# Optimization experiments

Measured on AMD Instinct MI355X. Metric: run time of the kernel, lower is better.

Reference implementation:

```python
import jax, jax.numpy as jnp
import numpy as np

B, T, IN, H, GAT_HEADS, MHA_HEADS, C = 32, 512, 128, 256, 4, 4, 8
OUT = H // GAT_HEADS          # 64, GAT per-head out_features
HD = H // MHA_HEADS           # 64, MHA head dim
ALPHA = 0.2                   # LeakyReLU slope
EPS = 1e-5                    # LayerNorm eps


def setup_inputs() -> dict:
    key = jax.random.key(0)
    ks = iter(jax.random.split(key, 32))
    def rn(shape, scale=0.05):
        return jax.random.normal(next(ks), shape, dtype=jnp.float32) * scale
    return {
        "x": jax.random.normal(next(ks), (B, T, IN), dtype=jnp.float32),
        # GRU layer 0 / 1 (PyTorch gate order r,z,n)
        "gru_W_ih0": rn((3 * H, IN)), "gru_W_hh0": rn((3 * H, H)),
        "gru_b_ih0": rn((3 * H,)), "gru_b_hh0": rn((3 * H,)),
        "gru_W_ih1": rn((3 * H, H)), "gru_W_hh1": rn((3 * H, H)),
        "gru_b_ih1": rn((3 * H,)), "gru_b_hh1": rn((3 * H,)),
        # GAT: per-head W [H,OUT] and additive attention vector a [2*OUT]
        "gat_W": rn((GAT_HEADS, H, OUT)), "gat_a": rn((GAT_HEADS, 2 * OUT)),
        "ln_g": jnp.ones((H,), jnp.float32), "ln_b": jnp.zeros((H,), jnp.float32),
        # MHA packed in-proj (q,k,v) + out-proj
        "mha_in_w": rn((3 * H, H)), "mha_in_b": rn((3 * H,)),
        "mha_out_w": rn((H, H)), "mha_out_b": rn((H,)),
        "fc1_w": rn((H // 2, H)), "fc1_b": rn((H // 2,)),
        "fc2_w": rn((C, H // 2)), "fc2_b": rn((C,)),
    }


def _gru_layer(x, W_ih, W_hh, b_ih, b_hh):
    # x: [B,T,D] -> hidden states [B,T,H]; PyTorch GRU cell math, gates r,z,n
    xp = jnp.einsum('btd,gd->btg', x, W_ih) + b_ih  # precompute input proj [B,T,3H]
    Hh = W_hh.shape[1]
    def step(h, xp_t):
        g = h @ W_hh.T + b_hh
        xr, xz, xn = jnp.split(xp_t, 3, axis=-1)
        hr, hz, hn = jnp.split(g, 3, axis=-1)
        r = jax.nn.sigmoid(xr + hr)
        z = jax.nn.sigmoid(xz + hz)
        n = jnp.tanh(xn + r * hn)
        h_new = (1.0 - z) * n + z * h
        return h_new, h_new
    h0 = jnp.zeros((x.shape[0], Hh), x.dtype)
    _, hs = jax.lax.scan(step, h0, jnp.swapaxes(xp, 0, 1))
    return jnp.swapaxes(hs, 0, 1)


def _gat_head(h_in, W, a):
    # Additive attention decomposed: e_ij = leakyrelu(a1.h_i + a2.h_j)
    # (exactly equals matmul(cat[h_i,h_j], a) without the [B,T,T,2*OUT] tensor)
    h = h_in @ W                       # [B,T,OUT]
    f_src = h @ a[:OUT]                # [B,T]
    f_dst = h @ a[OUT:]                # [B,T]
    e = jax.nn.leaky_relu(f_src[:, :, None] + f_dst[:, None, :], ALPHA)  # [B,T,T]
    attn = jax.nn.softmax(e, axis=-1)  # dropout is identity in eval mode
    return jnp.einsum('bij,bjd->bid', attn, h)


def _layer_norm(x, g, b):
    mu = x.mean(-1, keepdims=True)
    var = jnp.mean((x - mu) ** 2, -1, keepdims=True)
    return (x - mu) * jax.lax.rsqrt(var + EPS) * g + b


def _forward(x, gru_W_ih0, gru_W_hh0, gru_b_ih0, gru_b_hh0,
             gru_W_ih1, gru_W_hh1, gru_b_ih1, gru_b_hh1,
             gat_W, gat_a, ln_g, ln_b,
             mha_in_w, mha_in_b, mha_out_w, mha_out_b,
             fc1_w, fc1_b, fc2_w, fc2_b):
    g = _gru_layer(x, gru_W_ih0, gru_W_hh0, gru_b_ih0, gru_b_hh0)
    g = _gru_layer(g, gru_W_ih1, gru_W_hh1, gru_b_ih1, gru_b_hh1)  # [B,T,H]
    gat_out = jnp.concatenate([_gat_head(g, gat_W[i], gat_a[i]) for i in range(GAT_HEADS)], axis=-1)
    y = _layer_norm(g + gat_out, ln_g, ln_b)
    # Multihead self-attention (4 heads, eval-mode dropout = identity)
    qkv = y @ mha_in_w.T + mha_in_b
    q, k, v = jnp.split(qkv, 3, axis=-1)
    def split_heads(t):
        return t.reshape(t.shape[0], t.shape[1], MHA_HEADS, HD).transpose(0, 2, 1, 3)
    q, k, v = split_heads(q), split_heads(k), split_heads(v)
    scores = jnp.einsum('bhqd,bhkd->bhqk', q, k) / jnp.sqrt(jnp.float32(HD))
    attn = jax.nn.softmax(scores, axis=-1)
    ctx = jnp.einsum('bhqk,bhkd->bhqd', attn, v)
    ctx = ctx.transpose(0, 2, 1, 3).reshape(y.shape[0], y.shape[1], H)
    attn_out = ctx @ mha_out_w.T + mha_out_b
    pooled = attn_out.mean(axis=1)                    # [B,H]
    hid = jax.nn.relu(pooled @ fc1_w.T + fc1_b)
    return hid @ fc2_w.T + fc2_b                      # [B,C]


def reference(x, gru_W_ih0, gru_W_hh0, gru_b_ih0, gru_b_hh0,
              gru_W_ih1, gru_W_hh1, gru_b_ih1, gru_b_hh1,
              gat_W, gat_a, ln_g, ln_b,
              mha_in_w, mha_in_b, mha_out_w, mha_out_b,
              fc1_w, fc1_b, fc2_w, fc2_b):
    return _forward(x, gru_W_ih0, gru_W_hh0, gru_b_ih0, gru_b_hh0,
                    gru_W_ih1, gru_W_hh1, gru_b_ih1, gru_b_hh1,
                    gat_W, gat_a, ln_g, ln_b,
                    mha_in_w, mha_in_b, mha_out_w, mha_out_b,
                    fc1_w, fc1_b, fc2_w, fc2_b)
```

## Files before the change

kernel.cpp:

```cpp
#include <hip/hip_runtime.h>
#include <math.h>

#define BB 32
#define TT 512
#define INF_ 128
#define HH 256
#define H3 768
#define NHEADS 4
#define HDIM 64

typedef _Float16 half_t;
typedef half_t half2_t __attribute__((ext_vector_type(2)));
typedef half_t half4_t __attribute__((ext_vector_type(4)));
typedef half_t f16x8 __attribute__((ext_vector_type(8)));
typedef float f32x4 __attribute__((ext_vector_type(4)));

#if defined(__has_builtin)
#if __has_builtin(__builtin_amdgcn_fdot2)
#define FDOT2(a, b, c) __builtin_amdgcn_fdot2((a), (b), (c), false)
#endif
#endif
#ifndef FDOT2
#define FDOT2(a, b, c) fmaf((float)(a).x, (float)(b).x, fmaf((float)(a).y, (float)(b).y, (c)))
#endif

#define BCH(x) __builtin_bit_cast(half2_t, x)
#define PKH(a, b) __builtin_bit_cast(unsigned, half2_t{(half_t)(a), (half_t)(b)})

__device__ __forceinline__ float wsum(float v) {
#pragma unroll
  for (int o = 32; o > 0; o >>= 1) v += __shfl_xor(v, o, 64);
  return v;
}
__device__ __forceinline__ float wmax(float v) {
#pragma unroll
  for (int o = 32; o > 0; o >>= 1) v = fmaxf(v, __shfl_xor(v, o, 64));
  return v;
}

__global__ void castk(const float* __restrict__ s, half_t* __restrict__ d, int n) {
  int i = (blockIdx.x * 256 + threadIdx.x) * 4;
  if (i < n) {
    float4 v = *(const float4*)(s + i);
    half4_t o = {(half_t)v.x, (half_t)v.y, (half_t)v.z, (half_t)v.w};
    *(half4_t*)(d + i) = o;
  }
}

__global__ __launch_bounds__(256) void gemm_f16(
    const half_t* __restrict__ A, const half_t* __restrict__ B,
    const float* __restrict__ bias, float* __restrict__ C,
    int M, int N, int K) {
  __shared__ __align__(16) half_t As[128][40];
  __shared__ __align__(16) half_t Bs[64][40];
  const int tid = threadIdx.x;
  const int wave = tid >> 6, lane = tid & 63;
  const int m0 = blockIdx.y * 128, n0 = blockIdx.x * 64;
  const int mrow = lane & 15, quad = lane >> 4;
  f32x4 acc00 = {0.f, 0.f, 0.f, 0.f}, acc01 = acc00, acc02 = acc00, acc03 = acc00;
  f32x4 acc10 = acc00, acc11 = acc00, acc12 = acc00, acc13 = acc00;
  for (int k0 = 0; k0 < K; k0 += 32) {
    __syncthreads();
#pragma unroll
    for (int u = 0; u < 2; ++u) {
      int idx = tid + u * 256;
      int row = idx >> 2, seg = idx & 3;
      *(f16x8*)&As[row][seg * 8] =
          *(const f16x8*)&A[(size_t)(m0 + row) * K + k0 + seg * 8];
    }
    {
      int row = tid >> 2, seg = tid & 3;
      *(f16x8*)&Bs[row][seg * 8] =
          *(const f16x8*)&B[(size_t)(n0 + row) * K + k0 + seg * 8];
    }
    __syncthreads();
    f16x8 af0 = *(const f16x8*)&As[wave * 32 + mrow][quad * 8];
    f16x8 af1 = *(const f16x8*)&As[wave * 32 + 16 + mrow][quad * 8];
    f16x8 bf0 = *(const f16x8*)&Bs[mrow][quad * 8];
    f16x8 bf1 = *(const f16x8*)&Bs[16 + mrow][quad * 8];
    f16x8 bf2 = *(const f16x8*)&Bs[32 + mrow][quad * 8];
    f16x8 bf3 = *(const f16x8*)&Bs[48 + mrow][quad * 8];
    acc00 = __builtin_amdgcn_mfma_f32_16x16x32_f16(af0, bf0, acc00, 0, 0, 0);
    acc01 = __builtin_amdgcn_mfma_f32_16x16x32_f16(af0, bf1, acc01, 0, 0, 0);
    acc02 = __builtin_amdgcn_mfma_f32_16x16x32_f16(af0, bf2, acc02, 0, 0, 0);
    acc03 = __builtin_amdgcn_mfma_f32_16x16x32_f16(af0, bf3, acc03, 0, 0, 0);
    acc10 = __builtin_amdgcn_mfma_f32_16x16x32_f16(af1, bf0, acc10, 0, 0, 0);
    acc11 = __builtin_amdgcn_mfma_f32_16x16x32_f16(af1, bf1, acc11, 0, 0, 0);
    acc12 = __builtin_amdgcn_mfma_f32_16x16x32_f16(af1, bf2, acc12, 0, 0, 0);
    acc13 = __builtin_amdgcn_mfma_f32_16x16x32_f16(af1, bf3, acc13, 0, 0, 0);
  }
  float bv0 = bias ? bias[n0 + mrow] : 0.f;
  float bv1 = bias ? bias[n0 + 16 + mrow] : 0.f;
  float bv2 = bias ? bias[n0 + 32 + mrow] : 0.f;
  float bv3 = bias ? bias[n0 + 48 + mrow] : 0.f;
  const int rb = m0 + wave * 32 + quad * 4;
#pragma unroll
  for (int r = 0; r < 4; ++r) {
    float* c0 = C + (size_t)(rb + r) * N + n0;
    c0[mrow] = acc00[r] + bv0;
    c0[16 + mrow] = acc01[r] + bv1;
    c0[32 + mrow] = acc02[r] + bv2;
    c0[48 + mrow] = acc03[r] + bv3;
    float* c1 = C + (size_t)(rb + 16 + r) * N + n0;
    c1[mrow] = acc10[r] + bv0;
    c1[16 + mrow] = acc11[r] + bv1;
    c1[32 + mrow] = acc12[r] + bv2;
    c1[48 + mrow] = acc13[r] + bv3;
  }
}

#define LDW(g, p, a, b, i)                             \
  {                                                    \
    float4 v = (p)[i];                                 \
    g##a = half2_t{(half_t)v.x, (half_t)v.y};          \
    g##b = half2_t{(half_t)v.z, (half_t)v.w};          \
  }
#define LDW28(g, p)                                                        \
  LDW(g, p, 0, 1, 0) LDW(g, p, 2, 3, 1) LDW(g, p, 4, 5, 2)                 \
  LDW(g, p, 6, 7, 3) LDW(g, p, 8, 9, 4) LDW(g, p, 10, 11, 5)               \
  LDW(g, p, 12, 13, 6) LDW(g, p, 14, 15, 7) LDW(g, p, 16, 17, 8)           \
  LDW(g, p, 18, 19, 9) LDW(g, p, 20, 21, 10) LDW(g, p, 22, 23, 11)         \
  LDW(g, p, 24, 25, 12) LDW(g, p, 26, 27, 13) LDW(g, p, 28, 29, 14)        \
  LDW(g, p, 30, 31, 15) LDW(g, p, 32, 33, 16) LDW(g, p, 34, 35, 17)        \
  LDW(g, p, 36, 37, 18) LDW(g, p, 38, 39, 19) LDW(g, p, 40, 41, 20)        \
  LDW(g, p, 42, 43, 21) LDW(g, p, 44, 45, 22) LDW(g, p, 46, 47, 23)        \
  LDW(g, p, 48, 49, 24) LDW(g, p, 50, 51, 25) LDW(g, p, 52, 53, 26)        \
  LDW(g, p, 54, 55, 27)

#define DECL56(g)                                                          \
  half2_t g##0, g##1, g##2, g##3, g##4, g##5, g##6, g##7, g##8, g##9,      \
      g##10, g##11, g##12, g##13, g##14, g##15, g##16, g##17, g##18,       \
      g##19, g##20, g##21, g##22, g##23, g##24, g##25, g##26, g##27,       \
      g##28, g##29, g##30, g##31, g##32, g##33, g##34, g##35, g##36,       \
      g##37, g##38, g##39, g##40, g##41, g##42, g##43, g##44, g##45,       \
      g##46, g##47, g##48, g##49, g##50, g##51, g##52, g##53, g##54, g##55;

#define CHA(c8, a0, a1, a2, a3)                                            \
  {                                                                        \
    float4 v = hp4[c8];                                                    \
    uint4 nv = WSq[((c8)-1) * 512 + tid];                                  \
    half2_t t0 = __builtin_bit_cast(half2_t, v.x);                         \
    half2_t t1 = __builtin_bit_cast(half2_t, v.y);                         \
    half2_t t2 = __builtin_bit_cast(half2_t, v.z);                         \
    half2_t t3 = __builtin_bit_cast(half2_t, v.w);                         \
    ar = FDOT2(wr##a0, t0, ar); az = FDOT2(wz##a0, t0, az); an = FDOT2(BCH(nv.x), t0, an); \
    ar = FDOT2(wr##a1, t1, ar); az = FDOT2(wz##a1, t1, az); an = FDOT2(BCH(nv.y), t1, an); \
    ar = FDOT2(wr##a2, t2, ar); az = FDOT2(wz##a2, t2, az); an = FDOT2(BCH(nv.z), t2, an); \
    ar = FDOT2(wr##a3, t3, ar); az = FDOT2(wz##a3, t3, az); an = FDOT2(BCH(nv.w), t3, an); \
  }

#define CHB(c8)                                                            \
  {                                                                        \
    float4 v = hp4[c8];                                                    \
    uint4 nv = WSq[((c8)-1) * 512 + tid];                                  \
    uint4 rv = WSq[(15 + ((c8)-14)) * 512 + tid];                          \
    uint4 zv = WSq[(17 + ((c8)-14)) * 512 + tid];                          \
    half2_t t0 = __builtin_bit_cast(half2_t, v.x);                         \
    half2_t t1 = __builtin_bit_cast(half2_t, v.y);                         \
    half2_t t2 = __builtin_bit_cast(half2_t, v.z);                         \
    half2_t t3 = __builtin_bit_cast(half2_t, v.w);                         \
    ar = FDOT2(BCH(rv.x), t0, ar); az = FDOT2(BCH(zv.x), t0, az); an = FDOT2(BCH(nv.x), t0, an); \
    ar = FDOT2(BCH(rv.y), t1, ar); az = FDOT2(BCH(zv.y), t1, az); an = FDOT2(BCH(nv.y), t1, an); \
    ar = FDOT2(BCH(rv.z), t2, ar); az = FDOT2(BCH(zv.z), t2, az); an = FDOT2(BCH(nv.z), t2, an); \
    ar = FDOT2(BCH(rv.w), t3, ar); az = FDOT2(BCH(zv.w), t3, az); an = FDOT2(BCH(nv.w), t3, an); \
  }

__global__ __launch_bounds__(512) void gru_layer(
    const float* __restrict__ xp, const float* __restrict__ Whh,
    const float* __restrict__ bhh, float* __restrict__ out,
    half_t* __restrict__ out16) {
  __shared__ __align__(16) uint4 WSq[19 * 512];
  __shared__ __align__(16) half_t hs[2][2][144];
  const int tid = threadIdx.x;
  const int kh = tid & 1, j = tid >> 1;
  const int b = blockIdx.x;
  DECL56(wr)
  DECL56(wz)
  half2_t wn0, wn1, wn2, wn3;
  {
    const float4* pr = (const float4*)(Whh + (size_t)j * HH + kh * 128);
    const float4* pz = (const float4*)(Whh + (size_t)(HH + j) * HH + kh * 128);
    const float4* pn = (const float4*)(Whh + (size_t)(2 * HH + j) * HH + kh * 128);
    LDW28(wr, pr)
    LDW28(wz, pz)
    LDW(wn, pn, 0, 1, 0)
    LDW(wn, pn, 2, 3, 1)
  }
  {
    const float* rowN = Whh + (size_t)(2 * HH + j) * HH + kh * 128;
    const float* rowR = Whh + (size_t)j * HH + kh * 128;
    const float* rowZ = Whh + (size_t)(HH + j) * HH + kh * 128;
#pragma unroll
    for (int sg = 0; sg < 15; ++sg) {
      float2 g0 = *(const float2*)(rowN + (4 * sg + 4) * 2);
      float2 g1 = *(const float2*)(rowN + (4 * sg + 5) * 2);
      float2 g2 = *(const float2*)(rowN + (4 * sg + 6) * 2);
      float2 g3 = *(const float2*)(rowN + (4 * sg + 7) * 2);
      WSq[sg * 512 + tid] =
          uint4{PKH(g0.x, g0.y), PKH(g1.x, g1.y), PKH(g2.x, g2.y), PKH(g3.x, g3.y)};
    }
#pragma unroll
    for (int sg = 0; sg < 2; ++sg) {
      float2 g0 = *(const float2*)(rowR + (56 + 4 * sg) * 2);
      float2 g1 = *(const float2*)(rowR + (57 + 4 * sg) * 2);
      float2 g2 = *(const float2*)(rowR + (58 + 4 * sg) * 2);
      float2 g3 = *(const float2*)(rowR + (59 + 4 * sg) * 2);
      WSq[(15 + sg) * 512 + tid] =
          uint4{PKH(g0.x, g0.y), PKH(g1.x, g1.y), PKH(g2.x, g2.y), PKH(g3.x, g3.y)};
    }
#pragma unroll
    for (int sg = 0; sg < 2; ++sg) {
      float2 g0 = *(const float2*)(rowZ + (56 + 4 * sg) * 2);
      float2 g1 = *(const float2*)(rowZ + (57 + 4 * sg) * 2);
      float2 g2 = *(const float2*)(rowZ + (58 + 4 * sg) * 2);
      float2 g3 = *(const float2*)(rowZ + (59 + 4 * sg) * 2);
      WSq[(17 + sg) * 512 + tid] =
          uint4{PKH(g0.x, g0.y), PKH(g1.x, g1.y), PKH(g2.x, g2.y), PKH(g3.x, g3.y)};
    }
  }
  const float br = bhh[j], bz = bhh[HH + j], bn = bhh[2 * HH + j];
  for (int i = tid; i < 288; i += 512) ((unsigned*)hs)[i] = 0u;
  __syncthreads();
  float hprev = 0.f;
  const float* xrow = xp + (size_t)b * TT * H3;
  float* orow = out + (size_t)b * TT * HH;
  half_t* orow16 = out16 + (size_t)b * TT * HH;
  for (int t = 0; t < TT; ++t) {
    float xr = xrow[j], xz = xrow[HH + j], xn = xrow[2 * HH + j];
    const float4* hp4 = (const float4*)&hs[t & 1][kh][0];
    float ar = 0.f, az = 0.f, an = 0.f;
    {
      float4 v = hp4[0];
      half2_t t0 = __builtin_bit_cast(half2_t, v.x);
      half2_t t1 = __builtin_bit_cast(half2_t, v.y);
      half2_t t2 = __builtin_bit_cast(half2_t, v.z);
      half2_t t3 = __builtin_bit_cast(half2_t, v.w);
      ar = FDOT2(wr0, t0, ar); az = FDOT2(wz0, t0, az); an = FDOT2(wn0, t0, an);
      ar = FDOT2(wr1, t1, ar); az = FDOT2(wz1, t1, az); an = FDOT2(wn1, t1, an);
      ar = FDOT2(wr2, t2, ar); az = FDOT2(wz2, t2, az); an = FDOT2(wn2, t2, an);
      ar = FDOT2(wr3, t3, ar); az = FDOT2(wz3, t3, az); an = FDOT2(wn3, t3, an);
    }
    CHA(1, 4, 5, 6, 7)
    CHA(2, 8, 9, 10, 11)
    CHA(3, 12, 13, 14, 15)
    CHA(4, 16, 17, 18, 19)
    CHA(5, 20, 21, 22, 23)
    CHA(6, 24, 25, 26, 27)
    CHA(7, 28, 29, 30, 31)
    CHA(8, 32, 33, 34, 35)
    CHA(9, 36, 37, 38, 39)
    CHA(10, 40, 41, 42, 43)
    CHA(11, 44, 45, 46, 47)
    CHA(12, 48, 49, 50, 51)
    CHA(13, 52, 53, 54, 55)
    CHB(14)
    CHB(15)
    ar += __shfl_xor(ar, 1);
    az += __shfl_xor(az, 1);
    an += __shfl_xor(an, 1);
    float rg = 1.f / (1.f + __expf(-(xr + ar + br)));
    float zg = 1.f / (1.f + __expf(-(xz + az + bz)));
    float ng = 2.f / (1.f + __expf(-2.f * (xn + rg * (an + bn)))) - 1.f;
    float hnew = (1.f - zg) * ng + zg * hprev;
    hprev = hnew;
    float hpart = __shfl_xor(hnew, 2);
    if ((tid & 3) == 0) {
      half2_t pk;
      pk.x = (half_t)hnew;
      pk.y = (half_t)hpart;
      *(half2_t*)&hs[(t + 1) & 1][j >> 7][j & 127] = pk;
    }
    if (kh == 0) {
      orow[j] = hnew;
      orow16[j] = (half_t)hnew;
    }
    __syncthreads();
    xrow += H3;
    orow += HH;
    orow16 += HH;
  }
}

__global__ void gat_wt(const float* __restrict__ W, half_t* __restrict__ Wt) {
  int idx = blockIdx.x * 256 + threadIdx.x;
  int col = idx >> 8, k = idx & 255;
  Wt[idx] = (half_t)W[((size_t)((col >> 6) * HH + k)) * HDIM + (col & 63)];
}

__global__ void gat_fsd(const float* __restrict__ hgat, const float* __restrict__ a,
                        float* __restrict__ fsrc, float* __restrict__ fdst) {
  int b = blockIdx.x, hd = blockIdx.y, t = threadIdx.x;
  const float* hp = hgat + ((size_t)(b * TT + t)) * HH + hd * HDIM;
  const float* ap = a + hd * 2 * HDIM;
  float fs = 0.f, fd = 0.f;
#pragma unroll 4
  for (int d = 0; d < HDIM; ++d) {
    float hv = hp[d];
    fs += hv * ap[d];
    fd += hv * ap[HDIM + d];
  }
  fsrc[(b * NHEADS + hd) * TT + t] = fs;
  fdst[(b * NHEADS + hd) * TT + t] = fd;
}

__global__ __launch_bounds__(256) void gat_attn(
    const float* __restrict__ hgat, const float* __restrict__ fsrc,
    const float* __restrict__ fdst, float* __restrict__ out) {
  __shared__ __align__(16) float Ht[128][64];
  __shared__ __align__(16) float fd[128];
  __shared__ __align__(16) float pq[4][128][8];
  const int tid = threadIdx.x, wave = tid >> 6, lane = tid & 63;
  const int hd = blockIdx.y, b = blockIdx.z;
  const int i0 = blockIdx.x * 32 + wave * 8;
  const float* fs = fsrc + (size_t)(b * NHEADS + hd) * TT;
  const float* fdp = fdst + (size_t)(b * NHEADS + hd) * TT;
  float m[8], l[8], acc[8], fi[8];
#pragma unroll
  for (int q = 0; q < 8; ++q) { m[q] = -1e30f; l[q] = 0.f; acc[q] = 0.f; fi[q] = fs[i0 + q]; }
  for (int jt = 0; jt < TT; jt += 128) {
#pragma unroll
    for (int u = 0; u < 8; ++u) {
      int idx = tid + u * 256;
      int jj = idx >> 4, dq = (idx & 15) * 4;
      *(float4*)&Ht[jj][dq] =
          *(const float4*)&hgat[((size_t)(b * TT + jt + jj)) * HH + hd * HDIM + dq];
    }
    if (tid < 128) fd[tid] = fdp[jt + tid];
    __syncthreads();
#pragma unroll
    for (int q = 0; q < 8; ++q) {
      float e0 = fi[q] + fd[lane];      e0 = (e0 > 0.f) ? e0 : 0.2f * e0;
      float e1 = fi[q] + fd[lane + 64]; e1 = (e1 > 0.f) ? e1 : 0.2f * e1;
      float mn = fmaxf(m[q], wmax(fmaxf(e0, e1)));
      float corr = __expf(m[q] - mn);
      float p0 = __expf(e0 - mn), p1 = __expf(e1 - mn);
      l[q] = l[q] * corr + wsum(p0 + p1);
      m[q] = mn;
      acc[q] *= corr;
      pq[wave][lane][q] = p0;
      pq[wave][lane + 64][q] = p1;
    }
#pragma unroll 4
    for (int jj = 0; jj < 128; ++jj) {
      float4 pa = *(const float4*)&pq[wave][jj][0];
      float4 pb = *(const float4*)&pq[wave][jj][4];
      float hv = Ht[jj][lane];
      acc[0] += pa.x * hv; acc[1] += pa.y * hv; acc[2] += pa.z * hv; acc[3] += pa.w * hv;
      acc[4] += pb.x * hv; acc[5] += pb.y * hv; acc[6] += pb.z * hv; acc[7] += pb.w * hv;
    }
    __syncthreads();
  }
#pragma unroll
  for (int q = 0; q < 8; ++q)
    out[((size_t)(b * TT + i0 + q)) * HH + hd * HDIM + lane] = acc[q] / l[q];
}

__global__ __launch_bounds__(256) void ln_res(
    const float* __restrict__ g, const float* __restrict__ gat,
    const float* __restrict__ gamma, const float* __restrict__ beta,
    half_t* __restrict__ y16) {
  int wave = threadIdx.x >> 6, lane = threadIdx.x & 63;
  size_t n = (size_t)blockIdx.x * 4 + wave;
  float4 v = ((const float4*)(g + n * HH))[lane];
  float4 w = ((const float4*)(gat + n * HH))[lane];
  v.x += w.x; v.y += w.y; v.z += w.z; v.w += w.w;
  float mu = wsum(v.x + v.y + v.z + v.w) * (1.f / 256.f);
  float dx = v.x - mu, dy = v.y - mu, dz = v.z - mu, dw = v.w - mu;
  float var = wsum(dx * dx + dy * dy + dz * dz + dw * dw) * (1.f / 256.f);
  float rstd = rsqrtf(var + 1e-5f);
  float4 gm = ((const float4*)gamma)[lane];
  float4 bt = ((const float4*)beta)[lane];
  half4_t o = {(half_t)(dx * rstd * gm.x + bt.x), (half_t)(dy * rstd * gm.y + bt.y),
               (half_t)(dz * rstd * gm.z + bt.z), (half_t)(dw * rstd * gm.w + bt.w)};
  ((half4_t*)(y16 + n * HH))[lane] = o;
}

__global__ __launch_bounds__(256) void mha_attn(const float* __restrict__ qkv,
                                                half_t* __restrict__ ctx16) {
  __shared__ __align__(16) float KV[8320];
  __shared__ __align__(16) float qq[4][64][8];
  __shared__ __align__(16) float pq[4][128][8];
  const int tid = threadIdx.x, wave = tid >> 6, lane = tid & 63;
  const int hd = blockIdx.y, b = blockIdx.z;
  const int i0 = blockIdx.x * 32 + wave * 8;
#pragma unroll
  for (int q = 0; q < 8; ++q)
    qq[wave][lane][q] = qkv[((size_t)(b * TT + i0 + q)) * H3 + hd * HDIM + lane];
  float m[8], l[8], acc[8];
#pragma unroll
  for (int q = 0; q < 8; ++q) { m[q] = -1e30f; l[q] = 0.f; acc[q] = 0.f; }
  for (int jt = 0; jt < TT; jt += 128) {
#pragma unroll
    for (int u = 0; u < 8; ++u) {
      int idx = tid + u * 256;
      int jj = idx >> 4, dq = (idx & 15) * 4;
      float4 kv = *(const float4*)&qkv[((size_t)(b * TT + jt + jj)) * H3 + HH + hd * HDIM + dq];
      KV[(dq + 0) * 130 + jj] = kv.x;
      KV[(dq + 1) * 130 + jj] = kv.y;
      KV[(dq + 2) * 130 + jj] = kv.z;
      KV[(dq + 3) * 130 + jj] = kv.w;
    }
    __syncthreads();
    float e0[8] = {}, e1[8] = {};
#pragma unroll 8
    for (int dd = 0; dd < 64; ++dd) {
      float4 qa = *(const float4*)&qq[wave][dd][0];
      float4 qb = *(const float4*)&qq[wave][dd][4];
      float k0 = KV[dd * 130 + lane], k1 = KV[dd * 130 + 64 + lane];
      e0[0] += qa.x * k0; e0[1] += qa.y * k0; e0[2] += qa.z * k0; e0[3] += qa.w * k0;
      e0[4] += qb.x * k0; e0[5] += qb.y * k0; e0[6] += qb.z * k0; e0[7] += qb.w * k0;
      e1[0] += qa.x * k1; e1[1] += qa.y * k1; e1[2] += qa.z * k1; e1[3] += qa.w * k1;
      e1[4] += qb.x * k1; e1[5] += qb.y * k1; e1[6] += qb.z * k1; e1[7] += qb.w * k1;
    }
    __syncthreads();
#pragma unroll
    for (int u = 0; u < 8; ++u) {
      int idx = tid + u * 256;
      int jj = idx >> 4, dq = (idx & 15) * 4;
      *(float4*)&KV[jj * 64 + dq] =
          *(const float4*)&qkv[((size_t)(b * TT + jt + jj)) * H3 + 2 * HH + hd * HDIM + dq];
    }
#pragma unroll
    for (int q = 0; q < 8; ++q) {
      float s0 = e0[q] * 0.125f, s1 = e1[q] * 0.125f;
      float mn = fmaxf(m[q], wmax(fmaxf(s0, s1)));
      float corr = __expf(m[q] - mn);
      float p0 = __expf(s0 - mn), p1 = __expf(s1 - mn);
      l[q] = l[q] * corr + wsum(p0 + p1);
      m[q] = mn;
      acc[q] *= corr;
      pq[wave][lane][q] = p0;
      pq[wave][lane + 64][q] = p1;
    }
    __syncthreads();
#pragma unroll 4
    for (int jj = 0; jj < 128; ++jj) {
      float4 pa = *(const float4*)&pq[wave][jj][0];
      float4 pb = *(const float4*)&pq[wave][jj][4];
      float hv = KV[jj * 64 + lane];
      acc[0] += pa.x * hv; acc[1] += pa.y * hv; acc[2] += pa.z * hv; acc[3] += pa.w * hv;
      acc[4] += pb.x * hv; acc[5] += pb.y * hv; acc[6] += pb.z * hv; acc[7] += pb.w * hv;
    }
    __syncthreads();
  }
#pragma unroll
  for (int q = 0; q < 8; ++q)
    ctx16[((size_t)(b * TT + i0 + q)) * HH + hd * HDIM + lane] = (half_t)(acc[q] / l[q]);
}

__global__ void mean_pool(const float* __restrict__ x, float* __restrict__ out) {
  int b = blockIdx.x, j = threadIdx.x;
  const float* p = x + (size_t)b * TT * HH + j;
  float s = 0.f;
  for (int t = 0; t < TT; ++t) s += p[(size_t)t * HH];
  out[b * HH + j] = s * (1.f / 512.f);
}

__global__ void fc1_k(const float* __restrict__ pooled, const float* __restrict__ w,
                      const float* __restrict__ bias, float* __restrict__ hid) {
  int b = blockIdx.x, o = threadIdx.x;
  const float* pp = pooled + b * HH;
  const float* wp = w + o * HH;
  float s = 0.f;
#pragma unroll 4
  for (int k = 0; k < HH; ++k) s += pp[k] * wp[k];
  hid[b * 128 + o] = fmaxf(s + bias[o], 0.f);
}

__global__ void fc2_k(const float* __restrict__ hid, const float* __restrict__ w,
                      const float* __restrict__ bias, float* __restrict__ out) {
  int t = threadIdx.x;
  int mm = t >> 3, c = t & 7;
  const float* hp = hid + mm * 128;
  const float* wp = w + c * 128;
  float s = 0.f;
#pragma unroll 4
  for (int k = 0; k < 128; ++k) s += hp[k] * wp[k];
  out[mm * 8 + c] = s + bias[c];
}

extern "C" void kernel_launch(void* const* d_in, const int* in_sizes, int n_in,
                              void* d_out, int out_size, void* d_ws, size_t ws_size,
                              hipStream_t stream) {
  (void)in_sizes; (void)n_in; (void)out_size; (void)ws_size;
  const float* x    = (const float*)d_in[0];
  const float* Wih0 = (const float*)d_in[1];
  const float* Whh0 = (const float*)d_in[2];
  const float* bih0 = (const float*)d_in[3];
  const float* bhh0 = (const float*)d_in[4];
  const float* Wih1 = (const float*)d_in[5];
  const float* Whh1 = (const float*)d_in[6];
  const float* bih1 = (const float*)d_in[7];
  const float* bhh1 = (const float*)d_in[8];
  const float* gatW = (const float*)d_in[9];
  const float* gatA = (const float*)d_in[10];
  const float* lng  = (const float*)d_in[11];
  const float* lnb  = (const float*)d_in[12];
  const float* inw  = (const float*)d_in[13];
  const float* inb  = (const float*)d_in[14];
  const float* outw = (const float*)d_in[15];
  const float* outb = (const float*)d_in[16];
  const float* f1w  = (const float*)d_in[17];
  const float* f1b  = (const float*)d_in[18];
  const float* f2w  = (const float*)d_in[19];
  const float* f2b  = (const float*)d_in[20];
  float* out = (float*)d_out;
  float* ws = (float*)d_ws;

  float* XPA   = ws;
  float* G0    = ws + 12582912;
  float* G1    = G0 + 4194304;
  float* Yb    = G1 + 4194304;
  float* HGAT  = Yb + 4194304;
  float* GATWTf= HGAT + 4194304;
  float* FSRC  = GATWTf + 65536;
  float* FDST  = FSRC + 65536;
  float* POOL  = FDST + 65536;
  float* HIDb  = POOL + 8192;
  float* W16b  = HIDb + 4096;

  half_t* X16     = (half_t*)G1;
  half_t* G0_16   = (half_t*)Yb;
  half_t* G1_16   = (half_t*)(Yb + 2097152);
  half_t* CTX16   = (half_t*)HGAT;
  half_t* Y16     = (half_t*)(HGAT + 2097152);
  half_t* GATWT16 = (half_t*)GATWTf;
  half_t* W16ih0  = (half_t*)W16b;
  half_t* W16ih1  = (half_t*)(W16b + 49152);
  half_t* W16in   = (half_t*)(W16b + 49152 + 98304);
  half_t* W16out  = (half_t*)(W16b + 49152 + 98304 + 98304);

  castk<<<2048, 256, 0, stream>>>(x, X16, 2097152);
  castk<<<96, 256, 0, stream>>>(Wih0, W16ih0, 98304);
  castk<<<192, 256, 0, stream>>>(Wih1, W16ih1, 196608);
  castk<<<192, 256, 0, stream>>>(inw, W16in, 196608);
  castk<<<64, 256, 0, stream>>>(outw, W16out, 65536);
  gat_wt<<<256, 256, 0, stream>>>(gatW, GATWT16);
  gemm_f16<<<dim3(12, 128), 256, 0, stream>>>(X16, W16ih0, bih0, XPA, 16384, 768, 128);
  gru_layer<<<32, 512, 0, stream>>>(XPA, Whh0, bhh0, G0, G0_16);
  gemm_f16<<<dim3(12, 128), 256, 0, stream>>>(G0_16, W16ih1, bih1, XPA, 16384, 768, 256);
  gru_layer<<<32, 512, 0, stream>>>(XPA, Whh1, bhh1, G1, G1_16);
  gemm_f16<<<dim3(4, 128), 256, 0, stream>>>(G1_16, GATWT16, nullptr, HGAT, 16384, 256, 256);
  gat_fsd<<<dim3(32, 4), 512, 0, stream>>>(HGAT, gatA, FSRC, FDST);
  gat_attn<<<dim3(16, 4, 32), 256, 0, stream>>>(HGAT, FSRC, FDST, G0);
  ln_res<<<4096, 256, 0, stream>>>(G1, G0, lng, lnb, Y16);
  gemm_f16<<<dim3(12, 128), 256, 0, stream>>>(Y16, W16in, inb, XPA, 16384, 768, 256);
  mha_attn<<<dim3(16, 4, 32), 256, 0, stream>>>(XPA, CTX16);
  gemm_f16<<<dim3(4, 128), 256, 0, stream>>>(CTX16, W16out, outb, Yb, 16384, 256, 256);
  mean_pool<<<32, 256, 0, stream>>>(Yb, POOL);
  fc1_k<<<32, 128, 0, stream>>>(POOL, f1w, f1b, HIDb);
  fc2_k<<<1, 256, 0, stream>>>(HIDb, f2w, f2b, out);
}
```

Baseline: 1.917 ms.

## Remap GRU recurrence to two hidden units per thread with four-way K split

Each thread now computes two output hidden units over a quarter of the K dimension instead of one unit over half of K. This halves the hidden-state LDS reads per FMA, since each h chunk feeds two rows of weights. The input-projection loads and gate math are restricted to one lane in four. In exchange it adds an extra shuffle-reduction stage, concentrates the transcendental work on fewer lanes, and changes which weights live in registers versus LDS, which raises register pressure.

```diff
diff --git a/kernel.cpp b/kernel.cpp
--- a/kernel.cpp
+++ b/kernel.cpp
@@ -115,164 +115,154 @@
     g##a = half2_t{(half_t)v.x, (half_t)v.y};          \
     g##b = half2_t{(half_t)v.z, (half_t)v.w};          \
   }
-#define LDW28(g, p)                                                        \
+#define LDWALL32(g, p)                                                     \
   LDW(g, p, 0, 1, 0) LDW(g, p, 2, 3, 1) LDW(g, p, 4, 5, 2)                 \
   LDW(g, p, 6, 7, 3) LDW(g, p, 8, 9, 4) LDW(g, p, 10, 11, 5)               \
   LDW(g, p, 12, 13, 6) LDW(g, p, 14, 15, 7) LDW(g, p, 16, 17, 8)           \
   LDW(g, p, 18, 19, 9) LDW(g, p, 20, 21, 10) LDW(g, p, 22, 23, 11)         \
   LDW(g, p, 24, 25, 12) LDW(g, p, 26, 27, 13) LDW(g, p, 28, 29, 14)        \
-  LDW(g, p, 30, 31, 15) LDW(g, p, 32, 33, 16) LDW(g, p, 34, 35, 17)        \
-  LDW(g, p, 36, 37, 18) LDW(g, p, 38, 39, 19) LDW(g, p, 40, 41, 20)        \
-  LDW(g, p, 42, 43, 21) LDW(g, p, 44, 45, 22) LDW(g, p, 46, 47, 23)        \
-  LDW(g, p, 48, 49, 24) LDW(g, p, 50, 51, 25) LDW(g, p, 52, 53, 26)        \
-  LDW(g, p, 54, 55, 27)
-
-#define DECL56(g)                                                          \
+  LDW(g, p, 30, 31, 15)
+#define LDWALL20(g, p)                                                     \
+  LDW(g, p, 0, 1, 0) LDW(g, p, 2, 3, 1) LDW(g, p, 4, 5, 2)                 \
+  LDW(g, p, 6, 7, 3) LDW(g, p, 8, 9, 4) LDW(g, p, 10, 11, 5)               \
+  LDW(g, p, 12, 13, 6) LDW(g, p, 14, 15, 7) LDW(g, p, 16, 17, 8)           \
+  LDW(g, p, 18, 19, 9)
+
+#define DECL32(g)                                                          \
   half2_t g##0, g##1, g##2, g##3, g##4, g##5, g##6, g##7, g##8, g##9,      \
       g##10, g##11, g##12, g##13, g##14, g##15, g##16, g##17, g##18,       \
       g##19, g##20, g##21, g##22, g##23, g##24, g##25, g##26, g##27,       \
-      g##28, g##29, g##30, g##31, g##32, g##33, g##34, g##35, g##36,       \
-      g##37, g##38, g##39, g##40, g##41, g##42, g##43, g##44, g##45,       \
-      g##46, g##47, g##48, g##49, g##50, g##51, g##52, g##53, g##54, g##55;
-
-#define CHA(c8, a0, a1, a2, a3)                                            \
+      g##28, g##29, g##30, g##31;
+#define DECL20(g)                                                          \
+  half2_t g##0, g##1, g##2, g##3, g##4, g##5, g##6, g##7, g##8, g##9,      \
+      g##10, g##11, g##12, g##13, g##14, g##15, g##16, g##17, g##18, g##19;
+
+#define CHR(i, a0, a1, a2, a3)                                             \
   {                                                                        \
-    float4 v = hp4[c8];                                                    \
-    uint4 nv = WSq[((c8)-1) * 512 + tid];                                  \
+    float4 v = hp4[i];                                                     \
+    uint4 n0v = WSq[(i) * 512 + tid];                                      \
+    uint4 n1v = WSq[(8 + (i)) * 512 + tid];                                \
     half2_t t0 = __builtin_bit_cast(half2_t, v.x);                         \
     half2_t t1 = __builtin_bit_cast(half2_t, v.y);                         \
     half2_t t2 = __builtin_bit_cast(half2_t, v.z);                         \
     half2_t t3 = __builtin_bit_cast(half2_t, v.w);                         \
-    ar = FDOT2(wr##a0, t0, ar); az = FDOT2(wz##a0, t0, az); an = FDOT2(BCH(nv.x), t0, an); \
-    ar = FDOT2(wr##a1, t1, ar); az = FDOT2(wz##a1, t1, az); an = FDOT2(BCH(nv.y), t1, an); \
-    ar = FDOT2(wr##a2, t2, ar); az = FDOT2(wz##a2, t2, az); an = FDOT2(BCH(nv.z), t2, an); \
-    ar = FDOT2(wr##a3, t3, ar); az = FDOT2(wz##a3, t3, az); an = FDOT2(BCH(nv.w), t3, an); \
-  }
-
-#define CHB(c8)                                                            \
+    ar0 = FDOT2(wr##a0, t0, ar0); az0 = FDOT2(wz##a0, t0, az0); an0 = FDOT2(BCH(n0v.x), t0, an0); \
+    ar1 = FDOT2(wa##a0, t0, ar1); az1 = FDOT2(wb##a0, t0, az1); an1 = FDOT2(BCH(n1v.x), t0, an1); \
+    ar0 = FDOT2(wr##a1, t1, ar0); az0 = FDOT2(wz##a1, t1, az0); an0 = FDOT2(BCH(n0v.y), t1, an0); \
+    ar1 = FDOT2(wa##a1, t1, ar1); az1 = FDOT2(wb##a1, t1, az1); an1 = FDOT2(BCH(n1v.y), t1, an1); \
+    ar0 = FDOT2(wr##a2, t2, ar0); az0 = FDOT2(wz##a2, t2, az0); an0 = FDOT2(BCH(n0v.z), t2, an0); \
+    ar1 = FDOT2(wa##a2, t2, ar1); az1 = FDOT2(wb##a2, t2, az1); an1 = FDOT2(BCH(n1v.z), t2, an1); \
+    ar0 = FDOT2(wr##a3, t3, ar0); az0 = FDOT2(wz##a3, t3, az0); an0 = FDOT2(BCH(n0v.w), t3, an0); \
+    ar1 = FDOT2(wa##a3, t3, ar1); az1 = FDOT2(wb##a3, t3, az1); an1 = FDOT2(BCH(n1v.w), t3, an1); \
+  }
+
+#define CHS(i, a0, a1, a2, a3, zg)                                         \
   {                                                                        \
-    float4 v = hp4[c8];                                                    \
-    uint4 nv = WSq[((c8)-1) * 512 + tid];                                  \
-    uint4 rv = WSq[(15 + ((c8)-14)) * 512 + tid];                          \
-    uint4 zv = WSq[(17 + ((c8)-14)) * 512 + tid];                          \
+    float4 v = hp4[i];                                                     \
+    uint4 n0v = WSq[(i) * 512 + tid];                                      \
+    uint4 n1v = WSq[(8 + (i)) * 512 + tid];                                \
+    uint4 z1v = WSq[(zg) * 512 + tid];                                     \
     half2_t t0 = __builtin_bit_cast(half2_t, v.x);                         \
     half2_t t1 = __builtin_bit_cast(half2_t, v.y);                         \
     half2_t t2 = __builtin_bit_cast(half2_t, v.z);                         \
     half2_t t3 = __builtin_bit_cast(half2_t, v.w);                         \
-    ar = FDOT2(BCH(rv.x), t0, ar); az = FDOT2(BCH(zv.x), t0, az); an = FDOT2(BCH(nv.x), t0, an); \
-    ar = FDOT2(BCH(rv.y), t1, ar); az = FDOT2(BCH(zv.y), t1, az); an = FDOT2(BCH(nv.y), t1, an); \
-    ar = FDOT2(BCH(rv.z), t2, ar); az = FDOT2(BCH(zv.z), t2, az); an = FDOT2(BCH(nv.z), t2, an); \
-    ar = FDOT2(BCH(rv.w), t3, ar); az = FDOT2(BCH(zv.w), t3, az); an = FDOT2(BCH(nv.w), t3, an); \
-  }
+    ar0 = FDOT2(wr##a0, t0, ar0); az0 = FDOT2(wz##a0, t0, az0); an0 = FDOT2(BCH(n0v.x), t0, an0); \
+    ar1 = FDOT2(wa##a0, t0, ar1); az1 = FDOT2(BCH(z1v.x), t0, az1); an1 = FDOT2(BCH(n1v.x), t0, an1); \
+    ar0 = FDOT2(wr##a1, t1, ar0); az0 = FDOT2(wz##a1, t1, az0); an0 = FDOT2(BCH(n0v.y), t1, an0); \
+    ar1 = FDOT2(wa##a1, t1, ar1); az1 = FDOT2(BCH(z1v.y), t1, az1); an1 = FDOT2(BCH(n1v.y), t1, an1); \
+    ar0 = FDOT2(wr##a2, t2, ar0); az0 = FDOT2(wz##a2, t2, az0); an0 = FDOT2(BCH(n0v.z), t2, an0); \
+    ar1 = FDOT2(wa##a2, t2, ar1); az1 = FDOT2(BCH(z1v.z), t2, az1); an1 = FDOT2(BCH(n1v.z), t2, an1); \
+    ar0 = FDOT2(wr##a3, t3, ar0); az0 = FDOT2(wz##a3, t3, az0); an0 = FDOT2(BCH(n0v.w), t3, an0); \
+    ar1 = FDOT2(wa##a3, t3, ar1); az1 = FDOT2(BCH(z1v.w), t3, az1); an1 = FDOT2(BCH(n1v.w), t3, an1); \
+  }
+
+__device__ __forceinline__ uint4 pk8(const float* p) {
+  float4 a = *(const float4*)p;
+  float4 b = *(const float4*)(p + 4);
+  return uint4{PKH(a.x, a.y), PKH(a.z, a.w), PKH(b.x, b.y), PKH(b.z, b.w)};
+}
 
 __global__ __launch_bounds__(512) void gru_layer(
     const float* __restrict__ xp, const float* __restrict__ Whh,
     const float* __restrict__ bhh, float* __restrict__ out,
     half_t* __restrict__ out16) {
   __shared__ __align__(16) uint4 WSq[19 * 512];
-  __shared__ __align__(16) half_t hs[2][2][144];
+  __shared__ __align__(16) half_t hs[2][4][72];
   const int tid = threadIdx.x;
-  const int kh = tid & 1, j = tid >> 1;
+  const int kq = tid & 3, j2 = tid >> 2;
+  const int j0 = 2 * j2;
   const int b = blockIdx.x;
-  DECL56(wr)
-  DECL56(wz)
-  half2_t wn0, wn1, wn2, wn3;
+  DECL32(wr)
+  DECL32(wa)
+  DECL32(wz)
+  DECL20(wb)
   {
-    const float4* pr = (const float4*)(Whh + (size_t)j * HH + kh * 128);
-    const float4* pz = (const float4*)(Whh + (size_t)(HH + j) * HH + kh * 128);
-    const float4* pn = (const float4*)(Whh + (size_t)(2 * HH + j) * HH + kh * 128);
-    LDW28(wr, pr)
-    LDW28(wz, pz)
-    LDW(wn, pn, 0, 1, 0)
-    LDW(wn, pn, 2, 3, 1)
+    const float4* pr0 = (const float4*)(Whh + (size_t)j0 * HH + kq * 64);
+    const float4* pr1 = (const float4*)(Whh + (size_t)(j0 + 1) * HH + kq * 64);
+    const float4* pz0 = (const float4*)(Whh + (size_t)(HH + j0) * HH + kq * 64);
+    const float4* pz1 = (const float4*)(Whh + (size_t)(HH + j0 + 1) * HH + kq * 64);
+    LDWALL32(wr, pr0)
+    LDWALL32(wa, pr1)
+    LDWALL32(wz, pz0)
+    LDWALL20(wb, pz1)
   }
   {
-    const float* rowN = Whh + (size_t)(2 * HH + j) * HH + kh * 128;
-    const float* rowR = Whh + (size_t)j * HH + kh * 128;
-    const float* rowZ = Whh + (size_t)(HH + j) * HH + kh * 128;
-#pragma unroll
-    for (int sg = 0; sg < 15; ++sg) {
-      float2 g0 = *(const float2*)(rowN + (4 * sg + 4) * 2);
-      float2 g1 = *(const float2*)(rowN + (4 * sg + 5) * 2);
-      float2 g2 = *(const float2*)(rowN + (4 * sg + 6) * 2);
-      float2 g3 = *(const float2*)(rowN + (4 * sg + 7) * 2);
-      WSq[sg * 512 + tid] =
-          uint4{PKH(g0.x, g0.y), PKH(g1.x, g1.y), PKH(g2.x, g2.y), PKH(g3.x, g3.y)};
-    }
-#pragma unroll
-    for (int sg = 0; sg < 2; ++sg) {
-      float2 g0 = *(const float2*)(rowR + (56 + 4 * sg) * 2);
-      float2 g1 = *(const float2*)(rowR + (57 + 4 * sg) * 2);
-      float2 g2 = *(const float2*)(rowR + (58 + 4 * sg) * 2);
-      float2 g3 = *(const float2*)(rowR + (59 + 4 * sg) * 2);
-      WSq[(15 + sg) * 512 + tid] =
-          uint4{PKH(g0.x, g0.y), PKH(g1.x, g1.y), PKH(g2.x, g2.y), PKH(g3.x, g3.y)};
-    }
-#pragma unroll
-    for (int sg = 0; sg < 2; ++sg) {
-      float2 g0 = *(const float2*)(rowZ + (56 + 4 * sg) * 2);
-      float2 g1 = *(const float2*)(rowZ + (57 + 4 * sg) * 2);
-      float2 g2 = *(const float2*)(rowZ + (58 + 4 * sg) * 2);
-      float2 g3 = *(const float2*)(rowZ + (59 + 4 * sg) * 2);
-      WSq[(17 + sg) * 512 + tid] =
-          uint4{PKH(g0.x, g0.y), PKH(g1.x, g1.y), PKH(g2.x, g2.y), PKH(g3.x, g3.y)};
-    }
-  }
-  const float br = bhh[j], bz = bhh[HH + j], bn = bhh[2 * HH + j];
+    const float* rowN0 = Whh + (size_t)(2 * HH + j0) * HH + kq * 64;
+    const float* rowN1 = Whh + (size_t)(2 * HH + j0 + 1) * HH + kq * 64;
+    const float* rowZ1 = Whh + (size_t)(HH + j0 + 1) * HH + kq * 64;
+#pragma unroll
+    for (int g = 0; g < 8; ++g) WSq[g * 512 + tid] = pk8(rowN0 + 8 * g);
+#pragma unroll
+    for (int g = 0; g < 8; ++g) WSq[(8 + g) * 512 + tid] = pk8(rowN1 + 8 * g);
+#pragma unroll
+    for (int g = 0; g < 3; ++g) WSq[(16 + g) * 512 + tid] = pk8(rowZ1 + 40 + 8 * g);
+  }
+  const float br0 = bhh[j0], br1 = bhh[j0 + 1];
+  const float bz0 = bhh[HH + j0], bz1 = bhh[HH + j0 + 1];
+  const float bn0 = bhh[2 * HH + j0], bn1 = bhh[2 * HH + j0 + 1];
   for (int i = tid; i < 288; i += 512) ((unsigned*)hs)[i] = 0u;
   __syncthreads();
-  float hprev = 0.f;
+  float hprev0 = 0.f, hprev1 = 0.f;
   const float* xrow = xp + (size_t)b * TT * H3;
   float* orow = out + (size_t)b * TT * HH;
   half_t* orow16 = out16 + (size_t)b * TT * HH;
   for (int t = 0; t < TT; ++t) {
-    float xr = xrow[j], xz = xrow[HH + j], xn = xrow[2 * HH + j];
-    const float4* hp4 = (const float4*)&hs[t & 1][kh][0];
-    float ar = 0.f, az = 0.f, an = 0.f;
-    {
-      float4 v = hp4[0];
-      half2_t t0 = __builtin_bit_cast(half2_t, v.x);
-      half2_t t1 = __builtin_bit_cast(half2_t, v.y);
-      half2_t t2 = __builtin_bit_cast(half2_t, v.z);
-      half2_t t3 = __builtin_bit_cast(half2_t, v.w);
-      ar = FDOT2(wr0, t0, ar); az = FDOT2(wz0, t0, az); an = FDOT2(wn0, t0, an);
-      ar = FDOT2(wr1, t1, ar); az = FDOT2(wz1, t1, az); an = FDOT2(wn1, t1, an);
-      ar = FDOT2(wr2, t2, ar); az = FDOT2(wz2, t2, az); an = FDOT2(wn2, t2, an);
-      ar = FDOT2(wr3, t3, ar); az = FDOT2(wz3, t3, az); an = FDOT2(wn3, t3, an);
-    }
-    CHA(1, 4, 5, 6, 7)
-    CHA(2, 8, 9, 10, 11)
-    CHA(3, 12, 13, 14, 15)
-    CHA(4, 16, 17, 18, 19)
-    CHA(5, 20, 21, 22, 23)
-    CHA(6, 24, 25, 26, 27)
-    CHA(7, 28, 29, 30, 31)
-    CHA(8, 32, 33, 34, 35)
-    CHA(9, 36, 37, 38, 39)
-    CHA(10, 40, 41, 42, 43)
-    CHA(11, 44, 45, 46, 47)
-    CHA(12, 48, 49, 50, 51)
-    CHA(13, 52, 53, 54, 55)
-    CHB(14)
-    CHB(15)
-    ar += __shfl_xor(ar, 1);
-    az += __shfl_xor(az, 1);
-    an += __shfl_xor(an, 1);
-    float rg = 1.f / (1.f + __expf(-(xr + ar + br)));
-    float zg = 1.f / (1.f + __expf(-(xz + az + bz)));
-    float ng = 2.f / (1.f + __expf(-2.f * (xn + rg * (an + bn)))) - 1.f;
-    float hnew = (1.f - zg) * ng + zg * hprev;
-    hprev = hnew;
-    float hpart = __shfl_xor(hnew, 2);
-    if ((tid & 3) == 0) {
+    const float4* hp4 = (const float4*)&hs[t & 1][kq][0];
+    float ar0 = 0.f, az0 = 0.f, an0 = 0.f, ar1 = 0.f, az1 = 0.f, an1 = 0.f;
+    CHR(0, 0, 1, 2, 3)
+    CHR(1, 4, 5, 6, 7)
+    CHR(2, 8, 9, 10, 11)
+    CHR(3, 12, 13, 14, 15)
+    CHR(4, 16, 17, 18, 19)
+    CHS(5, 20, 21, 22, 23, 16)
+    CHS(6, 24, 25, 26, 27, 17)
+    CHS(7, 28, 29, 30, 31, 18)
+    ar0 += __shfl_xor(ar0, 1); ar0 += __shfl_xor(ar0, 2);
+    az0 += __shfl_xor(az0, 1); az0 += __shfl_xor(az0, 2);
+    an0 += __shfl_xor(an0, 1); an0 += __shfl_xor(an0, 2);
+    ar1 += __shfl_xor(ar1, 1); ar1 += __shfl_xor(ar1, 2);
+    az1 += __shfl_xor(az1, 1); az1 += __shfl_xor(az1, 2);
+    an1 += __shfl_xor(an1, 1); an1 += __shfl_xor(an1, 2);
+    if (kq == 0) {
+      float2 xr2 = *(const float2*)(xrow + j0);
+      float2 xz2 = *(const float2*)(xrow + HH + j0);
+      float2 xn2 = *(const float2*)(xrow + 2 * HH + j0);
+      float rg0 = 1.f / (1.f + __expf(-(xr2.x + ar0 + br0)));
+      float zg0 = 1.f / (1.f + __expf(-(xz2.x + az0 + bz0)));
+      float ng0 = 2.f / (1.f + __expf(-2.f * (xn2.x + rg0 * (an0 + bn0)))) - 1.f;
+      float h0 = (1.f - zg0) * ng0 + zg0 * hprev0;
+      float rg1 = 1.f / (1.f + __expf(-(xr2.y + ar1 + br1)));
+      float zg1 = 1.f / (1.f + __expf(-(xz2.y + az1 + bz1)));
+      float ng1 = 2.f / (1.f + __expf(-2.f * (xn2.y + rg1 * (an1 + bn1)))) - 1.f;
+      float h1 = (1.f - zg1) * ng1 + zg1 * hprev1;
+      hprev0 = h0;
+      hprev1 = h1;
       half2_t pk;
-      pk.x = (half_t)hnew;
-      pk.y = (half_t)hpart;
-      *(half2_t*)&hs[(t + 1) & 1][j >> 7][j & 127] = pk;
-    }
-    if (kh == 0) {
-      orow[j] = hnew;
-      orow16[j] = (half_t)hnew;
+      pk.x = (half_t)h0;
+      pk.y = (half_t)h1;
+      *(half2_t*)&hs[(t + 1) & 1][j2 >> 5][j0 & 63] = pk;
+      *(float2*)(orow + j0) = float2{h0, h1};
+      *(half2_t*)(orow16 + j0) = pk;
     }
     __syncthreads();
     xrow += H3;
```

Result: slower. 2.432 ms (+26.9%).
